# Kernel optimization log

Measured on AMD Instinct MI355X. Metric: run time of the kernel, lower is better.

Reference implementation:

```python
import jax, jax.numpy as jnp
import numpy as np

ALPHA = 0.2          # LeakyReLU negative slope
NEG_INF = -9e15      # mask fill value used by the original module

def setup_inputs() -> dict:
    key = jax.random.key(0)
    k1, k2, k3, k4 = jax.random.split(key, 4)
    B, N, F_in, F_out = 8, 2048, 64, 64
    inp = jax.random.normal(k1, (B, N, F_in), dtype=jnp.float32)
    adj = jax.random.randint(k2, (B, N, N), 0, 2, dtype=jnp.int32)
    # Parameters (kaiming-normal-ish init)
    W = jax.random.normal(k3, (F_in, F_out), dtype=jnp.float32) * np.sqrt(2.0 / F_in)
    a = jax.random.normal(k4, (2 * F_out, 1), dtype=jnp.float32) * np.sqrt(2.0 / (2 * F_out))
    return {"inp": inp, "adj": adj, "W": W, "a": a}

def reference(inp, adj, W, a):
    # h: [B, N, F_out]
    h = jnp.matmul(inp, W)
    F_out = W.shape[1]
    a1 = a[:F_out, 0]   # [F_out]
    a2 = a[F_out:, 0]   # [F_out]
    # e[b,i,j] = leakyrelu(h[b,i]·a1 + h[b,j]·a2)  -- broadcasted, avoids O(N^2*2F) concat
    f1 = h @ a1         # [B, N]
    f2 = h @ a2         # [B, N]
    e = jax.nn.leaky_relu(f1[:, :, None] + f2[:, None, :], negative_slope=ALPHA)
    scores = jnp.where(adj > 0, e, NEG_INF)
    attention = jax.nn.softmax(scores, axis=-1)  # [B, N, N]
    # dropout omitted (deterministic eval-mode reference)
    h_prime = jnp.matmul(attention, h)           # [B, N, F_out]
    return jax.nn.elu(h_prime)                   # concat=True path
```

## Files before the change

### kernel.cpp

```cpp
#include <hip/hip_runtime.h>
#include <hip/hip_bf16.h>

#define ALPHA 0.2f

constexpr int B = 8, N = 2048, F = 64;

typedef __attribute__((ext_vector_type(8))) short bf16x8;
typedef __attribute__((ext_vector_type(16))) float f32x16;

__device__ __forceinline__ float lrelu(float x) { return fmaxf(x, ALPHA * x); }

__global__ __launch_bounds__(256) void k1_project(
    const float* __restrict__ inp, const float* __restrict__ W,
    const float* __restrict__ a,
    __hip_bfloat16* __restrict__ hT, float* __restrict__ f1, float* __restrict__ f2)
{
  __shared__ float Wl[64][64];
  __shared__ float inpl[32][64];
  __shared__ float red[32][8][2];
  __shared__ __hip_bfloat16 hl[32][64];
  __shared__ float al[128];

  const int tid = threadIdx.x;
  const int g0 = blockIdx.x * 32;
  const int b = g0 / N, i0 = g0 % N;

  #pragma unroll
  for (int m = 0; m < 4; ++m) {
    int off = m * 1024 + tid * 4;
    *(float4*)((float*)Wl + off) = *(const float4*)(W + off);
  }
  #pragma unroll
  for (int m = 0; m < 2; ++m) {
    int off = m * 1024 + tid * 4;
    *(float4*)((float*)inpl + off) = *(const float4*)(inp + (size_t)g0 * F + off);
  }
  if (tid < 128) al[tid] = a[tid];
  __syncthreads();

  const int r = tid >> 3, c0 = (tid & 7) * 8;
  float acc[8];
  #pragma unroll
  for (int c = 0; c < 8; ++c) acc[c] = 0.f;
  for (int k = 0; k < 64; ++k) {
    float v = inpl[r][k];
    #pragma unroll
    for (int c = 0; c < 8; ++c) acc[c] += v * Wl[k][c0 + c];
  }
  float p1 = 0.f, p2 = 0.f;
  unsigned short hb[8] __attribute__((aligned(16)));
  #pragma unroll
  for (int c = 0; c < 8; ++c) {
    p1 += acc[c] * al[c0 + c];
    p2 += acc[c] * al[64 + c0 + c];
    __hip_bfloat16 hv = __float2bfloat16(acc[c]);
    hb[c] = *(unsigned short*)&hv;
  }
  red[r][tid & 7][0] = p1;
  red[r][tid & 7][1] = p2;
  *(uint4*)&hl[r][c0] = *(uint4*)hb;
  __syncthreads();

  if (tid < 32) {
    float s1 = 0.f, s2 = 0.f;
    #pragma unroll
    for (int m = 0; m < 8; ++m) { s1 += red[tid][m][0]; s2 += red[tid][m][1]; }
    f1[g0 + tid] = s1;
    f2[g0 + tid] = s2;
  }
  const int c = tid >> 2, r8 = (tid & 3) * 8;
  unsigned short tb[8] __attribute__((aligned(16)));
  #pragma unroll
  for (int m = 0; m < 8; ++m) tb[m] = *(unsigned short*)&hl[r8 + m][c];
  *(uint4*)(hT + ((size_t)b * F + c) * N + i0 + r8) = *(uint4*)tb;
}

__global__ __launch_bounds__(256) void k2_f2max(const float* __restrict__ f2,
                                                float* __restrict__ f2max)
{
  __shared__ float s[256];
  const int b = blockIdx.x, tid = threadIdx.x;
  float m = -1e30f;
  for (int j = tid; j < N; j += 256) m = fmaxf(m, f2[b * N + j]);
  s[tid] = m;
  __syncthreads();
  for (int w = 128; w > 0; w >>= 1) {
    if (tid < w) s[tid] = fmaxf(s[tid], s[tid + w]);
    __syncthreads();
  }
  if (tid == 0) f2max[b] = s[0];
}

__global__ __launch_bounds__(256) void k3_attn(
    const int* __restrict__ adj, const __hip_bfloat16* __restrict__ hT,
    const float* __restrict__ f1, const float* __restrict__ f2,
    const float* __restrict__ f2max, float* __restrict__ out)
{
  constexpr int RT = 32, JT = 128;
  __shared__ __hip_bfloat16 Pl[RT][JT];
  __shared__ __hip_bfloat16 hTl[F][JT];
  __shared__ float rs[RT][8];
  __shared__ float rcp[RT];
  __shared__ float redt[2][32][32];

  const int tid = threadIdx.x;
  const int lane = tid & 63, wid = tid >> 6;
  const int ct = wid >> 1, kh = wid & 1;
  const int bi = blockIdx.x;
  const int b = bi / (N / RT);
  const int i0 = (bi % (N / RT)) * RT;

  const int r = tid >> 3, jc = (tid & 7) * 16;
  const float f1r = f1[b * N + i0 + r];
  const float Mr = lrelu(f1r + f2max[b]);

  const int* adjrow = adj + ((size_t)(b * N + i0 + r)) * N + jc;
  const float* f2row = f2 + b * N + jc;
  const int hc = tid >> 2, js = (tid & 3) * 32;
  const __hip_bfloat16* hrow = hT + ((size_t)b * F + hc) * N + js;

  const int swp = (r & 7) << 3;
  const int swh = (hc & 7) << 3;

  float rowsum = 0.f;
  f32x16 acc;
  #pragma unroll
  for (int q = 0; q < 16; ++q) acc[q] = 0.f;

  for (int t = 0; t < N / JT; ++t) {
    const int j0 = t * JT;
    int4 av[4]; float4 fv[4]; uint4 hv[4];
    #pragma unroll
    for (int m = 0; m < 4; ++m) av[m] = *(const int4*)(adjrow + j0 + m * 4);
    #pragma unroll
    for (int m = 0; m < 4; ++m) fv[m] = *(const float4*)(f2row + j0 + m * 4);
    #pragma unroll
    for (int m = 0; m < 4; ++m) hv[m] = *(const uint4*)(hrow + j0 + m * 8);

    unsigned short pb[16] __attribute__((aligned(16)));
    #pragma unroll
    for (int m = 0; m < 4; ++m) {
      const int* ai = (const int*)&av[m];
      const float* fe = (const float*)&fv[m];
      #pragma unroll
      for (int e = 0; e < 4; ++e) {
        float s = lrelu(f1r + fe[e]);
        float p = (ai[e] > 0) ? __expf(s - Mr) : 0.f;
        __hip_bfloat16 pbf = __float2bfloat16(p);
        rowsum += __bfloat162float(pbf);
        pb[m * 4 + e] = *(unsigned short*)&pbf;
      }
    }
    *(uint4*)&Pl[r][jc ^ swp]       = *(uint4*)&pb[0];
    *(uint4*)&Pl[r][(jc + 8) ^ swp] = *(uint4*)&pb[8];
    #pragma unroll
    for (int m = 0; m < 4; ++m)
      *(uint4*)&hTl[hc][(js + m * 8) ^ swh] = hv[m];
    __syncthreads();

    const int arow = lane & 31;
    const int bcol = ct * 32 + (lane & 31);
    const int klo = kh * 64 + ((lane >> 5) * 8);
    #pragma unroll
    for (int s = 0; s < 4; ++s) {
      const int ak = klo + s * 16;
      bf16x8 af = *(const bf16x8*)&Pl[arow][ak ^ ((arow & 7) << 3)];
      bf16x8 bf = *(const bf16x8*)&hTl[bcol][ak ^ ((bcol & 7) << 3)];
      asm volatile("v_mfma_f32_32x32x16_bf16 %0, %1, %2, %0"
                   : "+v"(acc) : "v"(af), "v"(bf));
    }
    __syncthreads();
  }

  rs[r][tid & 7] = rowsum;
  if (kh == 1) {
    #pragma unroll
    for (int q = 0; q < 16; ++q)
      redt[ct][(q & 3) + 8 * (q >> 2) + 4 * (lane >> 5)][lane & 31] = acc[q];
  }
  __syncthreads();
  if (tid < 32) {
    float s = 0.f;
    #pragma unroll
    for (int m = 0; m < 8; ++m) s += rs[tid][m];
    rcp[tid] = 1.0f / fmaxf(s, 1e-30f);
  }
  __syncthreads();
  if (kh == 0) {
    #pragma unroll
    for (int q = 0; q < 16; ++q) {
      const int row = (q & 3) + 8 * (q >> 2) + 4 * (lane >> 5);
      float v = (acc[q] + redt[ct][row][lane & 31]) * rcp[row];
      v = v > 0.f ? v : expm1f(v);
      out[((size_t)(b * N + i0 + row)) * F + ct * 32 + (lane & 31)] = v;
    }
  }
}

extern "C" void kernel_launch(void* const* d_in, const int* in_sizes, int n_in,
                              void* d_out, int out_size, void* d_ws, size_t ws_size,
                              hipStream_t stream) {
  const float* inp = (const float*)d_in[0];
  const int*   adj = (const int*)d_in[1];
  const float* W   = (const float*)d_in[2];
  const float* a   = (const float*)d_in[3];
  float* out = (float*)d_out;

  char* ws = (char*)d_ws;
  __hip_bfloat16* hT = (__hip_bfloat16*)ws;
  float* f1  = (float*)(ws + (size_t)B * F * N * sizeof(__hip_bfloat16));
  float* f2  = f1 + (size_t)B * N;
  float* f2m = f2 + (size_t)B * N;

  hipLaunchKernelGGL(k1_project, dim3(B * N / 32), dim3(256), 0, stream, inp, W, a, hT, f1, f2);
  hipLaunchKernelGGL(k2_f2max, dim3(B), dim3(256), 0, stream, f2, f2m);
  hipLaunchKernelGGL(k3_attn, dim3(B * N / 32), dim3(256), 0, stream, adj, hT, f1, f2, f2m, out);
}
```

Measured before the change: 58.41 us.

## Double-buffer attention tiles with async global-to-LDS loads and register prefetch

The attention kernel now keeps two LDS buffers for the probability tile and the hT tile. The next hT tile is streamed with global_load_lds directly into the spare buffer while MFMAs run on the current one. The next tile's adjacency and f2 values are prefetched into registers, and one barrier per iteration is removed. The projection kernel writes hT pre-swizzled so the direct-to-LDS copy lands in the conflict-avoiding layout, which doubles LDS use and adds register pressure in exchange for overlapping memory latency with compute.

```diff
diff --git a/kernel.cpp b/kernel.cpp
--- a/kernel.cpp
+++ b/kernel.cpp
@@ -72,7 +72,9 @@
   unsigned short tb[8] __attribute__((aligned(16)));
   #pragma unroll
   for (int m = 0; m < 8; ++m) tb[m] = *(unsigned short*)&hl[r8 + m][c];
-  *(uint4*)(hT + ((size_t)b * F + c) * N + i0 + r8) = *(uint4*)tb;
+  const int jb = i0 + r8;
+  const int jsw = (jb & ~127) | ((jb & 127) ^ ((c & 7) << 3));
+  *(uint4*)(hT + ((size_t)b * F + c) * N + jsw) = *(uint4*)tb;
 }
 
 __global__ __launch_bounds__(256) void k2_f2max(const float* __restrict__ f2,
@@ -96,11 +98,11 @@
     const float* __restrict__ f1, const float* __restrict__ f2,
     const float* __restrict__ f2max, float* __restrict__ out)
 {
-  constexpr int RT = 32, JT = 128;
-  __shared__ __hip_bfloat16 Pl[RT][JT];
-  __shared__ __hip_bfloat16 hTl[F][JT];
+  constexpr int RT = 32, JT = 128, NT = N / JT;
+  __shared__ __hip_bfloat16 Pl[2][RT][JT];
+  __shared__ __hip_bfloat16 Hl[2][F][JT];
   __shared__ float rs[RT][8];
-  __shared__ float rcp[RT];
+  __shared__ float rcp_s[RT];
   __shared__ float redt[2][32][32];
 
   const int tid = threadIdx.x;
@@ -116,26 +118,48 @@
 
   const int* adjrow = adj + ((size_t)(b * N + i0 + r)) * N + jc;
   const float* f2row = f2 + b * N + jc;
-  const int hc = tid >> 2, js = (tid & 3) * 32;
-  const __hip_bfloat16* hrow = hT + ((size_t)b * F + hc) * N + js;
-
   const int swp = (r & 7) << 3;
-  const int swh = (hc & 7) << 3;
+
+  const __hip_bfloat16* hsrc =
+      hT + ((size_t)b * F + (wid * 16 + (lane >> 4))) * N + (lane & 15) * 8;
 
   float rowsum = 0.f;
   f32x16 acc;
   #pragma unroll
   for (int q = 0; q < 16; ++q) acc[q] = 0.f;
 
-  for (int t = 0; t < N / JT; ++t) {
-    const int j0 = t * JT;
-    int4 av[4]; float4 fv[4]; uint4 hv[4];
-    #pragma unroll
-    for (int m = 0; m < 4; ++m) av[m] = *(const int4*)(adjrow + j0 + m * 4);
-    #pragma unroll
-    for (int m = 0; m < 4; ++m) fv[m] = *(const float4*)(f2row + j0 + m * 4);
-    #pragma unroll
-    for (int m = 0; m < 4; ++m) hv[m] = *(const uint4*)(hrow + j0 + m * 8);
+  #define STAGE_H(T, BUFI)                                                      \
+    do {                                                                        \
+      const __hip_bfloat16* s0_ = hsrc + (T) * JT;                              \
+      char* lb_ = (char*)(&Hl[(BUFI)][0][0]) + wid * 4096;                      \
+      _Pragma("unroll")                                                         \
+      for (int q_ = 0; q_ < 4; ++q_) {                                          \
+        __builtin_amdgcn_global_load_lds(                                       \
+            (const __attribute__((address_space(1))) void*)(s0_ + q_ * 4 * N),  \
+            (__attribute__((address_space(3))) void*)(lb_ + q_ * 1024),         \
+            16, 0, 0);                                                          \
+      }                                                                         \
+    } while (0)
+
+  int4 av[4]; float4 fv[4];
+  #pragma unroll
+  for (int m = 0; m < 4; ++m) {
+    av[m] = *(const int4*)(adjrow + m * 4);
+    fv[m] = *(const float4*)(f2row + m * 4);
+  }
+  STAGE_H(0, 0);
+
+  for (int t = 0; t < NT; ++t) {
+    const int buf = t & 1;
+    const bool more = (t + 1 < NT);
+    int4 avn[4]; float4 fvn[4];
+    if (more) {
+      #pragma unroll
+      for (int m = 0; m < 4; ++m) {
+        avn[m] = *(const int4*)(adjrow + (t + 1) * JT + m * 4);
+        fvn[m] = *(const float4*)(f2row + (t + 1) * JT + m * 4);
+      }
+    }
 
     unsigned short pb[16] __attribute__((aligned(16)));
     #pragma unroll
@@ -151,12 +175,12 @@
         pb[m * 4 + e] = *(unsigned short*)&pbf;
       }
     }
-    *(uint4*)&Pl[r][jc ^ swp]       = *(uint4*)&pb[0];
-    *(uint4*)&Pl[r][(jc + 8) ^ swp] = *(uint4*)&pb[8];
-    #pragma unroll
-    for (int m = 0; m < 4; ++m)
-      *(uint4*)&hTl[hc][(js + m * 8) ^ swh] = hv[m];
+    *(uint4*)&Pl[buf][r][jc ^ swp]       = *(uint4*)&pb[0];
+    *(uint4*)&Pl[buf][r][(jc + 8) ^ swp] = *(uint4*)&pb[8];
+
     __syncthreads();
+
+    if (more) STAGE_H(t + 1, buf ^ 1);
 
     const int arow = lane & 31;
     const int bcol = ct * 32 + (lane & 31);
@@ -164,13 +188,18 @@
     #pragma unroll
     for (int s = 0; s < 4; ++s) {
       const int ak = klo + s * 16;
-      bf16x8 af = *(const bf16x8*)&Pl[arow][ak ^ ((arow & 7) << 3)];
-      bf16x8 bf = *(const bf16x8*)&hTl[bcol][ak ^ ((bcol & 7) << 3)];
+      bf16x8 af  = *(const bf16x8*)&Pl[buf][arow][ak ^ ((arow & 7) << 3)];
+      bf16x8 bfr = *(const bf16x8*)&Hl[buf][bcol][ak ^ ((bcol & 7) << 3)];
       asm volatile("v_mfma_f32_32x32x16_bf16 %0, %1, %2, %0"
-                   : "+v"(acc) : "v"(af), "v"(bf));
-    }
-    __syncthreads();
-  }
+                   : "+v"(acc) : "v"(af), "v"(bfr));
+    }
+
+    if (more) {
+      #pragma unroll
+      for (int m = 0; m < 4; ++m) { av[m] = avn[m]; fv[m] = fvn[m]; }
+    }
+  }
+  #undef STAGE_H
 
   rs[r][tid & 7] = rowsum;
   if (kh == 1) {
@@ -183,14 +212,14 @@
     float s = 0.f;
     #pragma unroll
     for (int m = 0; m < 8; ++m) s += rs[tid][m];
-    rcp[tid] = 1.0f / fmaxf(s, 1e-30f);
+    rcp_s[tid] = 1.0f / fmaxf(s, 1e-30f);
   }
   __syncthreads();
   if (kh == 0) {
     #pragma unroll
     for (int q = 0; q < 16; ++q) {
       const int row = (q & 3) + 8 * (q >> 2) + 4 * (lane >> 5);
-      float v = (acc[q] + redt[ct][row][lane & 31]) * rcp[row];
+      float v = (acc[q] + redt[ct][row][lane & 31]) * rcp_s[row];
       v = v > 0.f ? v : expm1f(v);
       out[((size_t)(b * N + i0 + row)) * F + ct * 32 + (lane & 31)] = v;
     }
```

Result: slower. 60.31 us (+3.3%).
